# Optimization experiments

Measured on AMD Instinct MI355X. Metric: run time of the kernel, lower is better.

The kernel has to match this reference:

```python
import jax, jax.numpy as jnp
import numpy as np

N, T, D, H = 128, 128, 1024, 1024


def setup_inputs() -> dict:
    key = jax.random.key(0)
    ks = jax.random.split(key, 5)
    x = jax.random.normal(ks[0], (N, T, D), dtype=jnp.float32)
    A = jax.random.normal(ks[1], (N, H, 4, 4), dtype=jnp.float32)
    Wx = jax.random.normal(ks[2], (D, 4 * H), dtype=jnp.float32) / np.sqrt(D)
    Wh = jax.random.normal(ks[3], (H, 4 * H), dtype=jnp.float32) / np.sqrt(H)
    Wattn = jax.random.normal(ks[4], (H, 4 * H), dtype=jnp.float32) / np.sqrt(H)
    b = jnp.zeros((4 * H,), dtype=jnp.float32)
    return {"x": x, "A": A, "Wx": Wx, "Wh": Wh, "Wattn": Wattn, "b": b}


def reference(x, A, Wx, Wh, Wattn, b):
    n, t, d = x.shape
    h_dim = A.shape[1]
    scale = 1.0 / (h_dim ** 0.5)
    A_flat = A.reshape(n, h_dim, 16)            # (N, H, 16) flattened 4x4 grid
    h0 = A_flat.mean(axis=2)                    # mean-pooled feature init
    c0 = h0

    def step(carry, xt):
        h, c = carry
        # scaled dot-product attention over the 16 spatial positions
        scores = jnp.einsum('nh,nhp->np', h, A_flat) * scale   # (N, 16)
        w = jax.nn.softmax(scores, axis=-1)
        attn = jnp.einsum('nhp,np->nh', A_flat, w)             # (N, H)
        # fused gate pre-activations
        a = h @ Wh + xt @ Wx + attn @ Wattn + b                # (N, 4H)
        ai, af, ao, ag = jnp.split(a, 4, axis=1)
        i = jax.nn.sigmoid(ai)
        f = jax.nn.sigmoid(af)
        o = jax.nn.sigmoid(ao)
        g = jnp.tanh(ag)
        nc = f * c + i * g
        nh = o * jnp.tanh(nc)
        return (nh, nc), nh

    _, hs = jax.lax.scan(step, (h0, c0), jnp.transpose(x, (1, 0, 2)))
    return jnp.transpose(hs, (1, 0, 2))         # (N, T, H)
```

## Files before the change

kernel.cpp:

```cpp
#include <hip/hip_runtime.h>
#include <hip/hip_bf16.h>


typedef __bf16 bf16x8 __attribute__((ext_vector_type(8)));
typedef float f32x4 __attribute__((ext_vector_type(4)));

__device__ __forceinline__ unsigned short f2bf(float f) {
    unsigned int u = __float_as_uint(f);
    u += 0x7FFFu + ((u >> 16) & 1u);
    return (unsigned short)(u >> 16);
}
__device__ __forceinline__ float bf2f(unsigned short u) {
    return __uint_as_float(((unsigned int)u) << 16);
}
__device__ __forceinline__ float sigf(float x) { return 1.0f / (1.0f + __expf(-x)); }
__device__ __forceinline__ float tanhf_fast(float x) {
    const float t = __expf(-2.0f * fabsf(x));
    const float r = (1.0f - t) / (1.0f + t);
    return copysignf(r, x);
}

__global__ __launch_bounds__(256) void k_build_wtf2(
    const float* __restrict__ Wh, const float* __restrict__ Wx,
    unsigned short* __restrict__ WTf) {
    __shared__ float tile[64][65];
    const int cs2 = blockIdx.x;
    const int kq  = blockIdx.y;
    const int tid = threadIdx.x;
#pragma unroll
    for (int it = 0; it < 16; ++it) {
        int idx = it * 256 + tid;
        int kl = idx >> 6, cl = idx & 63;
        int col = cs2 * 64 + cl;
        int j = (col & 3) * 1024 + (col >> 2);
        int k = kq * 64 + kl;
        tile[kl][cl] = (k < 1024) ? Wh[(size_t)k * 4096 + j]
                                  : Wx[(size_t)(k - 1024) * 4096 + j];
    }
    __syncthreads();
#pragma unroll
    for (int it = 0; it < 2; ++it) {
        int slotid = it * 256 + tid;
        int l   = slotid & 63;
        int cf  = (slotid >> 6) & 1;
        int ksl = (slotid >> 7) & 1;
        int sl  = slotid >> 8;
        int s = cs2 * 2 + sl, ks = kq * 2 + ksl;
        int clocal = sl * 32 + cf * 16 + (l & 15);
        int klocal = ksl * 32 + ((l >> 4) << 3);
        unsigned short v[8];
#pragma unroll
        for (int i = 0; i < 8; ++i) v[i] = f2bf(tile[klocal + i][clocal]);
        *(int4*)&WTf[(size_t)(((s * 64 + ks) * 2 + cf) * 64 + l) * 8] = *(const int4*)v;
    }
}

__global__ __launch_bounds__(256) void k_build_wf(
    const float* __restrict__ W, unsigned short* __restrict__ WF) {
    __shared__ float tile[64][65];
    const int cs2 = blockIdx.x;
    const int kq  = blockIdx.y;
    const int tid = threadIdx.x;
#pragma unroll
    for (int it = 0; it < 16; ++it) {
        int idx = it * 256 + tid;
        int kl = idx >> 6, cl = idx & 63;
        int col = cs2 * 64 + cl;
        int j = (col & 3) * 1024 + (col >> 2);
        int k = kq * 64 + kl;
        tile[kl][cl] = W[(size_t)k * 4096 + j];
    }
    __syncthreads();
#pragma unroll
    for (int it = 0; it < 2; ++it) {
        int slotid = it * 256 + tid;
        int l   = slotid & 63;
        int cf  = (slotid >> 6) & 1;
        int ksl = (slotid >> 7) & 1;
        int sl  = slotid >> 8;
        int s = cs2 * 2 + sl, ks = kq * 2 + ksl;
        int clocal = sl * 32 + cf * 16 + (l & 15);
        int klocal = ksl * 32 + ((l >> 4) << 3);
        unsigned short v[8];
#pragma unroll
        for (int i = 0; i < 8; ++i) v[i] = f2bf(tile[klocal + i][clocal]);
        *(int4*)&WF[(size_t)(((s * 32 + ks) * 2 + cf) * 64 + l) * 8] = *(const int4*)v;
    }
}

__global__ __launch_bounds__(256) void k_pack_at(
    const float* __restrict__ Ag, unsigned short* __restrict__ ATf) {
    __shared__ unsigned short lds[1024][17];
    const int n = blockIdx.x;
    const int tid = threadIdx.x;
#pragma unroll
    for (int it = 0; it < 16; ++it) {
        int idx = it * 256 + tid;
        const float4 v = ((const float4*)(Ag + (size_t)n * 16384))[idx];
        int flat = idx * 4;
        int u = flat >> 4, p = flat & 15;
        lds[u][p + 0] = f2bf(v.x); lds[u][p + 1] = f2bf(v.y);
        lds[u][p + 2] = f2bf(v.z); lds[u][p + 3] = f2bf(v.w);
    }
    __syncthreads();
#pragma unroll
    for (int it = 0; it < 8; ++it) {
        int slot = it * 256 + tid;
        int kc = slot >> 6, l = slot & 63;
        int ubase = kc * 32 + ((l >> 4) << 3);
        int p = l & 15;
        unsigned short v[8];
#pragma unroll
        for (int i = 0; i < 8; ++i) v[i] = lds[ubase + i][p];
        *(int4*)&ATf[((size_t)n * 2048 + slot) * 8] = *(const int4*)v;
    }
}

__global__ __launch_bounds__(512) void k_aw_gemm(
    const unsigned short* __restrict__ ATf, const unsigned short* __restrict__ WAf,
    unsigned short* __restrict__ AW) {
    const int ng = blockIdx.x;
    const int ct = blockIdx.y;
    const int tid = threadIdx.x;
    const int lane = tid & 63, wave = tid >> 6;
    const int s = ct * 4 + (wave >> 1), cf = wave & 1;
    const int n0 = ng * 8;
    f32x4 acc[8] = {};
    const unsigned short* bp = WAf + ((size_t)((s * 32) * 2 + cf) * 64 + lane) * 8;
    const unsigned short* ap = ATf + ((size_t)n0 * 2048 + lane) * 8;
#pragma unroll 4
    for (int kc = 0; kc < 32; ++kc) {
        bf16x8 bf = *(const bf16x8*)(bp + (size_t)kc * 1024);
#pragma unroll
        for (int nn = 0; nn < 8; ++nn) {
            bf16x8 af = *(const bf16x8*)(ap + (size_t)nn * 16384 + (size_t)kc * 512);
            acc[nn] = __builtin_amdgcn_mfma_f32_16x16x32_bf16(af, bf, acc[nn], 0, 0, 0);
        }
    }
    const int col = ct * 128 + wave * 16 + (lane & 15);
    const int prow = (lane >> 4) << 2;
#pragma unroll
    for (int nn = 0; nn < 8; ++nn) {
        ushort4 st = make_ushort4(f2bf(acc[nn][0]), f2bf(acc[nn][1]),
                                  f2bf(acc[nn][2]), f2bf(acc[nn][3]));
        *(ushort4*)&AW[((size_t)(n0 + nn) * 4096 + col) * 16 + prow] = st;
    }
}

__global__ __launch_bounds__(512) void k_build_aw(
    const float* __restrict__ Wattn, const float* __restrict__ Ag,
    unsigned short* __restrict__ AW) {
    extern __shared__ float Alds[];
    const int jt = blockIdx.x;
    const int ng = blockIdx.y;
    const int tid = threadIdx.x;
    const int jl = tid & 127, pg = tid >> 7;
    const int jj = jt * 128 + jl;
    for (int nn = 0; nn < 16; ++nn) {
        const int n = ng * 16 + nn;
        __syncthreads();
#pragma unroll
        for (int q = 0; q < 8; ++q) {
            int idx = q * 512 + tid;
            ((float4*)Alds)[idx] = ((const float4*)(Ag + (size_t)n * 16384))[idx];
        }
        __syncthreads();
        f32x4 acc = {0.f, 0.f, 0.f, 0.f};
#pragma unroll 8
        for (int u = 0; u < 1024; ++u) {
            float wv = Wattn[(size_t)u * 4096 + jj];
            const float4 av = *(const float4*)&Alds[u * 16 + pg * 4];
            acc[0] += wv * av.x; acc[1] += wv * av.y;
            acc[2] += wv * av.z; acc[3] += wv * av.w;
        }
        const int g = jj >> 10, unit = jj & 1023;
        const int cre = unit * 4 + g;
        ushort4 st = make_ushort4(f2bf(acc[0]), f2bf(acc[1]), f2bf(acc[2]), f2bf(acc[3]));
        *(ushort4*)&AW[((size_t)n * 4096 + cre) * 16 + pg * 4] = st;
    }
}

__global__ __launch_bounds__(512) void k_init(
    const float* __restrict__ Ag, float* __restrict__ cst,
    unsigned short* __restrict__ hF0, float* __restrict__ sp) {
    const int n = blockIdx.x;
    const int t = threadIdx.x;
    float contrib[16];
#pragma unroll
    for (int p = 0; p < 16; ++p) contrib[p] = 0.f;
#pragma unroll
    for (int e = 0; e < 2; ++e) {
        const int u = t * 2 + e;
        const float4* ap = (const float4*)&Ag[((size_t)n * 1024 + u) * 16];
        float4 a0 = ap[0], a1 = ap[1], a2 = ap[2], a3 = ap[3];
        float s = a0.x + a0.y + a0.z + a0.w + a1.x + a1.y + a1.z + a1.w +
                  a2.x + a2.y + a2.z + a2.w + a3.x + a3.y + a3.z + a3.w;
        float h0 = s * (1.0f / 16.0f);
        cst[n * 1024 + u] = h0;
        const int rfg = n >> 4, kc = u >> 5, l = (n & 15) | (((u >> 3) & 3) << 4);
        hF0[(size_t)((rfg * 32 + kc) * 64 + l) * 8 + (u & 7)] = f2bf(h0);
        contrib[0]  += h0 * a0.x;  contrib[1]  += h0 * a0.y;
        contrib[2]  += h0 * a0.z;  contrib[3]  += h0 * a0.w;
        contrib[4]  += h0 * a1.x;  contrib[5]  += h0 * a1.y;
        contrib[6]  += h0 * a1.z;  contrib[7]  += h0 * a1.w;
        contrib[8]  += h0 * a2.x;  contrib[9]  += h0 * a2.y;
        contrib[10] += h0 * a2.z;  contrib[11] += h0 * a2.w;
        contrib[12] += h0 * a3.x;  contrib[13] += h0 * a3.y;
        contrib[14] += h0 * a3.z;  contrib[15] += h0 * a3.w;
    }
#pragma unroll
    for (int p = 0; p < 16; ++p) {
        contrib[p] += __shfl_xor(contrib[p], 1);
        contrib[p] += __shfl_xor(contrib[p], 2);
    }
    if ((t & 3) == 0) {
        const int slice = t >> 2;
        float4* dst = (float4*)&sp[(size_t)n * 4096 + slice * 16];
        dst[0] = make_float4(contrib[0], contrib[1], contrib[2], contrib[3]);
        dst[1] = make_float4(contrib[4], contrib[5], contrib[6], contrib[7]);
        dst[2] = make_float4(contrib[8], contrib[9], contrib[10], contrib[11]);
        dst[3] = make_float4(contrib[12], contrib[13], contrib[14], contrib[15]);
    }
    *(float4*)&sp[(size_t)n * 4096 + 2048 + t * 4] = make_float4(0.f, 0.f, 0.f, 0.f);
}

__global__ __launch_bounds__(512) void k_soft(
    const float* __restrict__ spin, float* __restrict__ w_ws,
    const float* __restrict__ x, unsigned short* __restrict__ xf, int ts) {
    __shared__ float sq[8][16];
    const int bid = blockIdx.x;
    const int tid = threadIdx.x;
    const int lane = tid & 63, wave = tid >> 6;
    const int n = bid * 8 + wave;
    f32x4 acc = {0.f, 0.f, 0.f, 0.f};
    const float4* base = (const float4*)(spin + (size_t)n * 4096);
#pragma unroll
    for (int it = 0; it < 16; ++it) {
        const float4 v = base[it * 64 + lane];
        acc[0] += v.x; acc[1] += v.y; acc[2] += v.z; acc[3] += v.w;
    }
#pragma unroll
    for (int m = 4; m <= 32; m <<= 1) {
        acc[0] += __shfl_xor(acc[0], m);
        acc[1] += __shfl_xor(acc[1], m);
        acc[2] += __shfl_xor(acc[2], m);
        acc[3] += __shfl_xor(acc[3], m);
    }
    if (lane < 4) *(f32x4*)&sq[wave][lane * 4] = acc;
    __syncthreads();
    if (lane < 16) {
        const float s = sq[wave][lane] * 0.03125f;
        float mx = s;
#pragma unroll
        for (int m = 1; m < 16; m <<= 1) mx = fmaxf(mx, __shfl_xor(mx, m));
        const float e = __expf(s - mx);
        float se = e;
#pragma unroll
        for (int m = 1; m < 16; m <<= 1) se += __shfl_xor(se, m);
        w_ws[n * 16 + lane] = e / se;
    }
#pragma unroll
    for (int it = 0; it < 2; ++it) {
        const int slot = it * 8192 + bid * 512 + tid;
        const int nn = slot >> 7, js = slot & 127, j0 = js * 8;
        const float4* xp = (const float4*)&x[((size_t)nn * 128 + ts) * 1024 + j0];
        float4 x0 = xp[0], x1 = xp[1];
        unsigned short v[8] = {f2bf(x0.x), f2bf(x0.y), f2bf(x0.z), f2bf(x0.w),
                               f2bf(x1.x), f2bf(x1.y), f2bf(x1.z), f2bf(x1.w)};
        const int rfg = nn >> 4, kc = j0 >> 5, l = (nn & 15) | (((j0 >> 3) & 3) << 4);
        *(int4*)&xf[(size_t)((rfg * 32 + kc) * 64 + l) * 8] = *(const int4*)v;
    }
}

__global__ __launch_bounds__(1024, 4) void k_step(
    const unsigned short* __restrict__ WTf, const unsigned short* __restrict__ AW,
    const unsigned short* __restrict__ hFin, unsigned short* __restrict__ hFout,
    const unsigned short* __restrict__ xf,
    const float* __restrict__ w_ws, float* __restrict__ sp,
    float* __restrict__ cst, const float* __restrict__ Ag,
    const float* __restrict__ bias4, float* __restrict__ out, int ts) {
    __shared__ float wlds[128][17];
    __shared__ f32x4 accred[16][64];
    const int bid0 = blockIdx.x;
    const int lid = (bid0 & 7) * 32 + (bid0 >> 3);
    const int cs32 = lid >> 1, rh = lid & 1;
    const int tid = threadIdx.x;
    const int lane = tid & 63, wave = tid >> 6;
    const int rf = wave >> 2, kh = (wave >> 1) & 1, cf = wave & 1;

#pragma unroll
    for (int it = 0; it < 2; ++it) {
        const int idx = it * 1024 + tid;
        wlds[idx >> 4][idx & 15] = w_ws[idx];
    }

    f32x4 acc = {0.f, 0.f, 0.f, 0.f};
    {
        const unsigned short* ap = (kh == 0 ? hFin : xf)
            + ((size_t)((rh * 4 + rf) * 32) * 64 + lane) * 8;
        const unsigned short* bp = WTf
            + ((size_t)(((cs32 * 64 + kh * 32) * 2) + cf) * 64 + lane) * 8;
        bf16x8 ar[8], br[8];
#pragma unroll
        for (int i = 0; i < 8; ++i) {
            ar[i] = *(const bf16x8*)(ap + (size_t)i * 512);
            br[i] = *(const bf16x8*)(bp + (size_t)i * 1024);
        }
#pragma unroll
        for (int kb = 0; kb < 32; ++kb) {
            bf16x8 a = ar[kb & 7], b = br[kb & 7];
            if (kb < 24) {
                ar[kb & 7] = *(const bf16x8*)(ap + (size_t)(kb + 8) * 512);
                br[kb & 7] = *(const bf16x8*)(bp + (size_t)(kb + 8) * 1024);
            }
            acc = __builtin_amdgcn_mfma_f32_16x16x32_bf16(a, b, acc, 0, 0, 0);
        }
    }

    const int lq = lane & 15, hi = lane >> 4;
    const int mycol = cs32 * 32 + cf * 16 + lq;
    const int u = mycol >> 2, g = mycol & 3;
    const int r0 = rh * 64 + rf * 16 + hi * 4;
    int4 aw0[2], aw1[2];
    float cold[2];
#pragma unroll
    for (int e = 0; e < 2; ++e) {
        const int r = r0 + kh * 2 + e;
        const int4* awv = (const int4*)&AW[((size_t)r * 4096 + mycol) * 16];
        aw0[e] = awv[0];
        aw1[e] = awv[1];
        cold[e] = cst[r * 1024 + u];
    }
    const float bias = bias4[g * 1024 + u];

    accred[wave][lane] = acc;
    __syncthreads();
    acc += accred[wave ^ 2][lane];

    float nhv[2];
#pragma unroll
    for (int e = 0; e < 2; ++e) {
        const int reg = kh * 2 + e;
        const int r = r0 + reg;
        union { int4 v; unsigned short us[8]; } a0u, a1u;
        a0u.v = aw0[e]; a1u.v = aw1[e];
        float aextra = 0.f;
#pragma unroll
        for (int p = 0; p < 8; ++p) aextra += wlds[r][p] * bf2f(a0u.us[p]);
#pragma unroll
        for (int p = 0; p < 8; ++p) aextra += wlds[r][8 + p] * bf2f(a1u.us[p]);
        float a = acc[reg] + bias + aextra;
        float v1 = __shfl_xor(a, 1);
        float v2 = __shfl_xor(a, 2);
        float v3 = __shfl_xor(a, 3);
        auto pick = [&](int m) { return m == 0 ? a : m == 1 ? v1 : m == 2 ? v2 : v3; };
        float ii = sigf(pick(g));
        float ff = sigf(pick(g ^ 1));
        float oo = sigf(pick(g ^ 2));
        float gg = tanhf_fast(pick(g ^ 3));
        const float nc = ff * cold[e] + ii * gg;
        const float nh = oo * tanhf_fast(nc);
        nhv[e] = nh;
        if (g == 0) {
            cst[r * 1024 + u] = nc;
        } else if (g == 1) {
            hFout[(size_t)(((r >> 4) * 32 + (u >> 5)) * 64 +
                           ((r & 15) | (((u >> 3) & 3) << 4))) * 8 + (u & 7)] = f2bf(nh);
        } else if (g == 3) {
            __builtin_nontemporal_store(nh, &out[((size_t)r * 128 + ts) * 1024 + u]);
        }
    }
    if ((lq & 3) == 2) {
#pragma unroll
        for (int e = 0; e < 2; ++e) {
            const int r = r0 + kh * 2 + e;
            const float nh = nhv[e];
            const float4* Ap = (const float4*)&Ag[((size_t)r * 1024 + u) * 16];
            float contrib[16];
#pragma unroll
            for (int q = 0; q < 4; ++q) {
                const float4 cv = Ap[q];
                contrib[q * 4 + 0] = nh * cv.x;
                contrib[q * 4 + 1] = nh * cv.y;
                contrib[q * 4 + 2] = nh * cv.z;
                contrib[q * 4 + 3] = nh * cv.w;
            }
#pragma unroll
            for (int p = 0; p < 16; ++p) {
                contrib[p] += __shfl_xor(contrib[p], 4);
                contrib[p] += __shfl_xor(contrib[p], 8);
            }
            if (lq == 2) {
                float4* dst = (float4*)&sp[((size_t)r * 256 + (cs32 * 2 + cf)) * 16];
                dst[0] = make_float4(contrib[0], contrib[1], contrib[2], contrib[3]);
                dst[1] = make_float4(contrib[4], contrib[5], contrib[6], contrib[7]);
                dst[2] = make_float4(contrib[8], contrib[9], contrib[10], contrib[11]);
                dst[3] = make_float4(contrib[12], contrib[13], contrib[14], contrib[15]);
            }
        }
    }
}

extern "C" void kernel_launch(void* const* d_in, const int* in_sizes, int n_in,
                              void* d_out, int out_size, void* d_ws, size_t ws_size,
                              hipStream_t stream) {
    const float* x     = (const float*)d_in[0];
    const float* A     = (const float*)d_in[1];
    const float* Wx    = (const float*)d_in[2];
    const float* Wh    = (const float*)d_in[3];
    const float* Wattn = (const float*)d_in[4];
    const float* b     = (const float*)d_in[5];
    float* out = (float*)d_out;

    char* ws = (char*)d_ws;
    unsigned short* WTf = (unsigned short*)(ws);
    unsigned short* AW  = (unsigned short*)(ws + 16777216);
    unsigned short* hF0 = (unsigned short*)(ws + 33554432);
    unsigned short* hF1 = (unsigned short*)(ws + 33816576);
    unsigned short* xf  = (unsigned short*)(ws + 34078720);
    float* cst   = (float*)(ws + 34603008);
    float* w_ws  = (float*)(ws + 35127296);
    float* sp    = (float*)(ws + 35143680);
    unsigned short* ATf = (unsigned short*)(ws + 33554432);
    unsigned short* WAf = (unsigned short*)(ws + 37748736);

    k_build_wtf2<<<dim3(64, 32), 256, 0, stream>>>(Wh, Wx, WTf);
    if (ws_size >= 46137344u) {
        k_build_wf<<<dim3(64, 16), 256, 0, stream>>>(Wattn, WAf);
        k_pack_at<<<128, 256, 0, stream>>>(A, ATf);
        k_aw_gemm<<<dim3(16, 32), 512, 0, stream>>>(ATf, WAf, AW);
    } else {
        k_build_aw<<<dim3(32, 8), 512, 65536, stream>>>(Wattn, A, AW);
    }
    k_init<<<128, 512, 0, stream>>>(A, cst, hF0, sp);

    for (int ts = 0; ts < 128; ++ts) {
        unsigned short* hin  = (ts & 1) ? hF1 : hF0;
        unsigned short* hout = (ts & 1) ? hF0 : hF1;
        k_soft<<<16, 512, 0, stream>>>(sp, w_ws, x, xf, ts);
        k_step<<<256, 1024, 0, stream>>>(WTf, AW, hin, hout, xf,
                                         w_ws, sp, cst, A, b, out, ts);
    }
}
```

Baseline: 2.834 ms.

## Compute attention scores via MFMA in softmax kernel instead of step partials

The attention scores h·A are no longer built from per-block partial sums written by the step kernel. The softmax kernel now computes them directly with bf16 MFMA, using a packed transposed A and the bf16 hidden state. This removes the step kernel's per-step read of A, its 16-way shuffle reductions and the partial-score writes. The step kernel is also retiled to 512-thread blocks on a grid twice as large, and the workspace is rearranged so the packed A persists through the loop. Scores now carry bf16 rounding of h and A instead of fp32 accumulation.

```diff
diff --git a/kernel.cpp b/kernel.cpp
--- a/kernel.cpp
+++ b/kernel.cpp
@@ -182,12 +182,9 @@
 
 __global__ __launch_bounds__(512) void k_init(
     const float* __restrict__ Ag, float* __restrict__ cst,
-    unsigned short* __restrict__ hF0, float* __restrict__ sp) {
+    unsigned short* __restrict__ hF0) {
     const int n = blockIdx.x;
     const int t = threadIdx.x;
-    float contrib[16];
-#pragma unroll
-    for (int p = 0; p < 16; ++p) contrib[p] = 0.f;
 #pragma unroll
     for (int e = 0; e < 2; ++e) {
         const int u = t * 2 + e;
@@ -199,54 +196,36 @@
         cst[n * 1024 + u] = h0;
         const int rfg = n >> 4, kc = u >> 5, l = (n & 15) | (((u >> 3) & 3) << 4);
         hF0[(size_t)((rfg * 32 + kc) * 64 + l) * 8 + (u & 7)] = f2bf(h0);
-        contrib[0]  += h0 * a0.x;  contrib[1]  += h0 * a0.y;
-        contrib[2]  += h0 * a0.z;  contrib[3]  += h0 * a0.w;
-        contrib[4]  += h0 * a1.x;  contrib[5]  += h0 * a1.y;
-        contrib[6]  += h0 * a1.z;  contrib[7]  += h0 * a1.w;
-        contrib[8]  += h0 * a2.x;  contrib[9]  += h0 * a2.y;
-        contrib[10] += h0 * a2.z;  contrib[11] += h0 * a2.w;
-        contrib[12] += h0 * a3.x;  contrib[13] += h0 * a3.y;
-        contrib[14] += h0 * a3.z;  contrib[15] += h0 * a3.w;
-    }
-#pragma unroll
-    for (int p = 0; p < 16; ++p) {
-        contrib[p] += __shfl_xor(contrib[p], 1);
-        contrib[p] += __shfl_xor(contrib[p], 2);
-    }
-    if ((t & 3) == 0) {
-        const int slice = t >> 2;
-        float4* dst = (float4*)&sp[(size_t)n * 4096 + slice * 16];
-        dst[0] = make_float4(contrib[0], contrib[1], contrib[2], contrib[3]);
-        dst[1] = make_float4(contrib[4], contrib[5], contrib[6], contrib[7]);
-        dst[2] = make_float4(contrib[8], contrib[9], contrib[10], contrib[11]);
-        dst[3] = make_float4(contrib[12], contrib[13], contrib[14], contrib[15]);
-    }
-    *(float4*)&sp[(size_t)n * 4096 + 2048 + t * 4] = make_float4(0.f, 0.f, 0.f, 0.f);
+    }
 }
 
 __global__ __launch_bounds__(512) void k_soft(
-    const float* __restrict__ spin, float* __restrict__ w_ws,
-    const float* __restrict__ x, unsigned short* __restrict__ xf, int ts) {
-    __shared__ float sq[8][16];
+    const unsigned short* __restrict__ ATf, const unsigned short* __restrict__ hF,
+    float* __restrict__ w_ws, const float* __restrict__ x,
+    unsigned short* __restrict__ xf, int ts) {
+    __shared__ float sq[8][20];
     const int bid = blockIdx.x;
     const int tid = threadIdx.x;
     const int lane = tid & 63, wave = tid >> 6;
     const int n = bid * 8 + wave;
+    const int hi = lane >> 4;
+
     f32x4 acc = {0.f, 0.f, 0.f, 0.f};
-    const float4* base = (const float4*)(spin + (size_t)n * 4096);
-#pragma unroll
-    for (int it = 0; it < 16; ++it) {
-        const float4 v = base[it * 64 + lane];
-        acc[0] += v.x; acc[1] += v.y; acc[2] += v.z; acc[3] += v.w;
-    }
-#pragma unroll
-    for (int m = 4; m <= 32; m <<= 1) {
-        acc[0] += __shfl_xor(acc[0], m);
-        acc[1] += __shfl_xor(acc[1], m);
-        acc[2] += __shfl_xor(acc[2], m);
-        acc[3] += __shfl_xor(acc[3], m);
-    }
-    if (lane < 4) *(f32x4*)&sq[wave][lane * 4] = acc;
+    {
+        const unsigned short* ap = ATf + ((size_t)n * 2048 + lane) * 8;
+        const unsigned short* bp = hF +
+            ((size_t)((n >> 4) * 32) * 64 + ((n & 15) | (hi << 4))) * 8;
+#pragma unroll 8
+        for (int kc = 0; kc < 32; ++kc) {
+            bf16x8 af = *(const bf16x8*)(ap + (size_t)kc * 512);
+            bf16x8 bf = *(const bf16x8*)(bp + (size_t)kc * 512);
+            acc = __builtin_amdgcn_mfma_f32_16x16x32_bf16(af, bf, acc, 0, 0, 0);
+        }
+    }
+    if ((lane & 15) == 0) {
+#pragma unroll
+        for (int reg = 0; reg < 4; ++reg) sq[wave][hi * 4 + reg] = acc[reg];
+    }
     __syncthreads();
     if (lane < 16) {
         const float s = sq[wave][lane] * 0.03125f;
@@ -272,34 +251,27 @@
     }
 }
 
-__global__ __launch_bounds__(1024, 4) void k_step(
+__global__ __launch_bounds__(512, 4) void k_step(
     const unsigned short* __restrict__ WTf, const unsigned short* __restrict__ AW,
     const unsigned short* __restrict__ hFin, unsigned short* __restrict__ hFout,
-    const unsigned short* __restrict__ xf,
-    const float* __restrict__ w_ws, float* __restrict__ sp,
-    float* __restrict__ cst, const float* __restrict__ Ag,
+    const unsigned short* __restrict__ xfin,
+    const float* __restrict__ w_ws, float* __restrict__ cst,
     const float* __restrict__ bias4, float* __restrict__ out, int ts) {
-    __shared__ float wlds[128][17];
-    __shared__ f32x4 accred[16][64];
+    __shared__ float wlds[64][17];
+    __shared__ float accred[2048];
     const int bid0 = blockIdx.x;
-    const int lid = (bid0 & 7) * 32 + (bid0 >> 3);
-    const int cs32 = lid >> 1, rh = lid & 1;
+    const int lid = (bid0 & 7) * 64 + (bid0 >> 3);
+    const int cs16 = lid >> 1, rh = lid & 1;
     const int tid = threadIdx.x;
     const int lane = tid & 63, wave = tid >> 6;
-    const int rf = wave >> 2, kh = (wave >> 1) & 1, cf = wave & 1;
-
-#pragma unroll
-    for (int it = 0; it < 2; ++it) {
-        const int idx = it * 1024 + tid;
-        wlds[idx >> 4][idx & 15] = w_ws[idx];
-    }
+    const int rf = wave >> 1, kh = wave & 1;
 
     f32x4 acc = {0.f, 0.f, 0.f, 0.f};
     {
-        const unsigned short* ap = (kh == 0 ? hFin : xf)
+        const unsigned short* ap = (kh == 0 ? hFin : xfin)
             + ((size_t)((rh * 4 + rf) * 32) * 64 + lane) * 8;
         const unsigned short* bp = WTf
-            + ((size_t)(((cs32 * 64 + kh * 32) * 2) + cf) * 64 + lane) * 8;
+            + ((size_t)((((cs16 >> 1) * 64 + kh * 32) * 2) + (cs16 & 1)) * 64 + lane) * 8;
         bf16x8 ar[8], br[8];
 #pragma unroll
         for (int i = 0; i < 8; ++i) {
@@ -317,38 +289,43 @@
         }
     }
 
-    const int lq = lane & 15, hi = lane >> 4;
-    const int mycol = cs32 * 32 + cf * 16 + lq;
+    const int lq = lane & 15;
+    const int hi = lane >> 4;
+    const int mycol = cs16 * 16 + lq;
     const int u = mycol >> 2, g = mycol & 3;
-    const int r0 = rh * 64 + rf * 16 + hi * 4;
     int4 aw0[2], aw1[2];
     float cold[2];
 #pragma unroll
     for (int e = 0; e < 2; ++e) {
-        const int r = r0 + kh * 2 + e;
+        const int reg = kh * 2 + e;
+        const int r = rh * 64 + rf * 16 + hi * 4 + reg;
         const int4* awv = (const int4*)&AW[((size_t)r * 4096 + mycol) * 16];
         aw0[e] = awv[0];
         aw1[e] = awv[1];
         cold[e] = cst[r * 1024 + u];
     }
+#pragma unroll
+    for (int it = 0; it < 2; ++it) {
+        const int idx = it * 512 + tid;
+        wlds[idx >> 4][idx & 15] = w_ws[(rh * 64 + (idx >> 4)) * 16 + (idx & 15)];
+    }
+    *(f32x4*)&accred[(wave * 64 + lane) * 4] = acc;
+    __syncthreads();
+    acc += *(const f32x4*)&accred[(((rf << 1) | (kh ^ 1)) * 64 + lane) * 4];
+
     const float bias = bias4[g * 1024 + u];
-
-    accred[wave][lane] = acc;
-    __syncthreads();
-    acc += accred[wave ^ 2][lane];
-
-    float nhv[2];
 #pragma unroll
     for (int e = 0; e < 2; ++e) {
         const int reg = kh * 2 + e;
-        const int r = r0 + reg;
+        const int r = rh * 64 + rf * 16 + hi * 4 + reg;
+        const int rl = rf * 16 + hi * 4 + reg;
         union { int4 v; unsigned short us[8]; } a0u, a1u;
         a0u.v = aw0[e]; a1u.v = aw1[e];
         float aextra = 0.f;
 #pragma unroll
-        for (int p = 0; p < 8; ++p) aextra += wlds[r][p] * bf2f(a0u.us[p]);
-#pragma unroll
-        for (int p = 0; p < 8; ++p) aextra += wlds[r][8 + p] * bf2f(a1u.us[p]);
+        for (int p = 0; p < 8; ++p) aextra += wlds[rl][p] * bf2f(a0u.us[p]);
+#pragma unroll
+        for (int p = 0; p < 8; ++p) aextra += wlds[rl][8 + p] * bf2f(a1u.us[p]);
         float a = acc[reg] + bias + aextra;
         float v1 = __shfl_xor(a, 1);
         float v2 = __shfl_xor(a, 2);
@@ -360,7 +337,6 @@
         float gg = tanhf_fast(pick(g ^ 3));
         const float nc = ff * cold[e] + ii * gg;
         const float nh = oo * tanhf_fast(nc);
-        nhv[e] = nh;
         if (g == 0) {
             cst[r * 1024 + u] = nc;
         } else if (g == 1) {
@@ -368,35 +344,6 @@
                            ((r & 15) | (((u >> 3) & 3) << 4))) * 8 + (u & 7)] = f2bf(nh);
         } else if (g == 3) {
             __builtin_nontemporal_store(nh, &out[((size_t)r * 128 + ts) * 1024 + u]);
-        }
-    }
-    if ((lq & 3) == 2) {
-#pragma unroll
-        for (int e = 0; e < 2; ++e) {
-            const int r = r0 + kh * 2 + e;
-            const float nh = nhv[e];
-            const float4* Ap = (const float4*)&Ag[((size_t)r * 1024 + u) * 16];
-            float contrib[16];
-#pragma unroll
-            for (int q = 0; q < 4; ++q) {
-                const float4 cv = Ap[q];
-                contrib[q * 4 + 0] = nh * cv.x;
-                contrib[q * 4 + 1] = nh * cv.y;
-                contrib[q * 4 + 2] = nh * cv.z;
-                contrib[q * 4 + 3] = nh * cv.w;
-            }
-#pragma unroll
-            for (int p = 0; p < 16; ++p) {
-                contrib[p] += __shfl_xor(contrib[p], 4);
-                contrib[p] += __shfl_xor(contrib[p], 8);
-            }
-            if (lq == 2) {
-                float4* dst = (float4*)&sp[((size_t)r * 256 + (cs32 * 2 + cf)) * 16];
-                dst[0] = make_float4(contrib[0], contrib[1], contrib[2], contrib[3]);
-                dst[1] = make_float4(contrib[4], contrib[5], contrib[6], contrib[7]);
-                dst[2] = make_float4(contrib[8], contrib[9], contrib[10], contrib[11]);
-                dst[3] = make_float4(contrib[12], contrib[13], contrib[14], contrib[15]);
-            }
         }
     }
 }
@@ -415,30 +362,29 @@
     char* ws = (char*)d_ws;
     unsigned short* WTf = (unsigned short*)(ws);
     unsigned short* AW  = (unsigned short*)(ws + 16777216);
-    unsigned short* hF0 = (unsigned short*)(ws + 33554432);
-    unsigned short* hF1 = (unsigned short*)(ws + 33816576);
-    unsigned short* xf  = (unsigned short*)(ws + 34078720);
-    float* cst   = (float*)(ws + 34603008);
-    float* w_ws  = (float*)(ws + 35127296);
-    float* sp    = (float*)(ws + 35143680);
     unsigned short* ATf = (unsigned short*)(ws + 33554432);
+    unsigned short* hF0 = (unsigned short*)(ws + 37748736);
+    unsigned short* hF1 = (unsigned short*)(ws + 38010880);
+    unsigned short* xf  = (unsigned short*)(ws + 38273024);
+    float* cst   = (float*)(ws + 38535168);
+    float* w_ws  = (float*)(ws + 39059456);
     unsigned short* WAf = (unsigned short*)(ws + 37748736);
 
     k_build_wtf2<<<dim3(64, 32), 256, 0, stream>>>(Wh, Wx, WTf);
+    k_pack_at<<<128, 256, 0, stream>>>(A, ATf);
     if (ws_size >= 46137344u) {
         k_build_wf<<<dim3(64, 16), 256, 0, stream>>>(Wattn, WAf);
-        k_pack_at<<<128, 256, 0, stream>>>(A, ATf);
         k_aw_gemm<<<dim3(16, 32), 512, 0, stream>>>(ATf, WAf, AW);
     } else {
         k_build_aw<<<dim3(32, 8), 512, 65536, stream>>>(Wattn, A, AW);
     }
-    k_init<<<128, 512, 0, stream>>>(A, cst, hF0, sp);
+    k_init<<<128, 512, 0, stream>>>(A, cst, hF0);
 
     for (int ts = 0; ts < 128; ++ts) {
         unsigned short* hin  = (ts & 1) ? hF1 : hF0;
         unsigned short* hout = (ts & 1) ? hF0 : hF1;
-        k_soft<<<16, 512, 0, stream>>>(sp, w_ws, x, xf, ts);
-        k_step<<<256, 1024, 0, stream>>>(WTf, AW, hin, hout, xf,
-                                         w_ws, sp, cst, A, b, out, ts);
-    }
-}
+        k_soft<<<16, 512, 0, stream>>>(ATf, hin, w_ws, x, xf, ts);
+        k_step<<<512, 512, 0, stream>>>(WTf, AW, hin, hout, xf,
+                                        w_ws, cst, b, out, ts);
+    }
+}
```

Measured after the change: 2.900 ms. 2.3% more time.
